# Performance work log

Measured on AMD Instinct MI355X. Metric: run time of the kernel, lower is better.

Reference implementation:

```python
import jax, jax.numpy as jnp
import numpy as np


def setup_inputs() -> dict:
    key = jax.random.key(0)
    k1, k2 = jax.random.split(key)
    B, D, H, W = 64, 64, 32, 32
    K = 1024
    z_e = jax.random.normal(k1, (B, D, H, W), dtype=jnp.float32)
    embedding = jax.random.normal(k2, (K, D), dtype=jnp.float32)
    return {"z_e": z_e, "embedding": embedding}


def reference(z_e, embedding):
    # Eval-mode forward of VectorQuantizer (EMA buffer updates are training-only state).
    B, D, H, W = z_e.shape
    K = embedding.shape[0]
    # (N, D) flattened encoder outputs, N = B*H*W
    flat = jnp.transpose(z_e, (0, 2, 3, 1)).reshape(-1, D)
    dist = (jnp.sum(flat * flat, axis=1, keepdims=True)
            + jnp.sum(embedding * embedding, axis=1)
            - 2.0 * flat @ embedding.T)  # (N, K)
    indices = jnp.argmin(dist, axis=1)  # (N,)
    z_q_flat = embedding[indices]  # (N, D) gather
    z_q = jnp.transpose(z_q_flat.reshape(B, H, W, D), (0, 3, 1, 2))
    # commitment loss: mse(z_e, sg(z_q))
    commitment_loss = jnp.mean((z_e - jax.lax.stop_gradient(z_q)) ** 2)
    # straight-through estimator
    z_q = z_e + jax.lax.stop_gradient(z_q - z_e)
    indices_bhw = indices.reshape(B, H, W)
    # fraction of codebook entries used this batch (jit-friendly unique count)
    used = jnp.zeros((K,), dtype=jnp.float32).at[indices].set(1.0)
    codebook_usage = jnp.sum(used) / K
    return z_q, commitment_loss, indices_bhw, codebook_usage
```

## Files before the change

kernel.cpp:

```cpp
#include <hip/hip_runtime.h>


#define DIMS 64
#define K_CODES 1024
#define N_QUERIES 65536
#define HW 1024
#define TOTAL_ELEMS 4194304
#define PLANE 4096

typedef __attribute__((ext_vector_type(8))) short v8s;
typedef __attribute__((ext_vector_type(4))) float f32x4;

__device__ inline unsigned short f2bf(float x) {
    union { float f; unsigned u; } v; v.f = x;
    unsigned r = v.u + 0x7fff + ((v.u >> 16) & 1);
    return (unsigned short)(r >> 16);
}
__device__ inline float bf2f(unsigned short h) {
    union { unsigned u; float f; } v; v.u = ((unsigned)h) << 16; return v.f;
}

__global__ void vq_prep(const float* __restrict__ emb, float* __restrict__ ws_norm,
                        int* __restrict__ ws_flags, float* __restrict__ ws_loss) {
    int k = blockIdx.x * 256 + threadIdx.x;
    const float4* row = (const float4*)(emb + k * DIMS);
    float s = 0.f;
#pragma unroll
    for (int i = 0; i < 16; ++i) {
        float4 v = row[i];
        s += v.x * v.x + v.y * v.y + v.z * v.z + v.w * v.w;
    }
    ws_norm[k] = s;
    ws_flags[k] = 0;
    if (k == 0) *ws_loss = 0.f;
}

#define MFMA16(A_, B_, C_) __builtin_amdgcn_mfma_f32_16x16x32_bf16(A_, B_, C_, 0, 0, 0)

__global__ __launch_bounds__(256, 2)
void vq_main(const float* __restrict__ z_e, const float* __restrict__ emb,
             const float* __restrict__ ws_norm, int* __restrict__ ws_flags,
             float* __restrict__ ws_loss, float* __restrict__ out) {
    __shared__ unsigned short ldsB[2][3 * PLANE];
    __shared__ int   fIdx[128];
    __shared__ float wsum[4];

    const int tid  = threadIdx.x;
    const int lane = tid & 63;
    const int wid  = tid >> 6;
    const int qbase = blockIdx.x * 128;
    const int b    = qbase >> 10;
    const int hwb  = qbase & (HW - 1);

    const int col  = lane & 15;
    const int qd   = lane >> 4;

    v8s afr[2][2][3];
    {
        const float* zb = z_e + b * (DIMS * HW);
#pragma unroll
        for (int rt = 0; rt < 2; ++rt) {
            int hwq = hwb + wid * 32 + rt * 16 + col;
#pragma unroll
            for (int kc = 0; kc < 2; ++kc) {
                int dbase = kc * 32 + qd * 8;
#pragma unroll
                for (int j = 0; j < 8; ++j) {
                    float x = zb[(dbase + j) * HW + hwq];
                    unsigned short h = f2bf(x);  float r1 = x - bf2f(h);
                    unsigned short m = f2bf(r1); float r2 = r1 - bf2f(m);
                    afr[rt][kc][0][j] = (short)h;
                    afr[rt][kc][1][j] = (short)m;
                    afr[rt][kc][2][j] = (short)f2bf(r2);
                }
            }
        }
    }

    float bestv[2][4];
    int   besti[2][4];
#pragma unroll
    for (int rt = 0; rt < 2; ++rt)
#pragma unroll
        for (int r = 0; r < 4; ++r) { bestv[rt][r] = 3.4e38f; besti[rt][r] = 0; }

    float4 regs[4];

    auto stage_loads = [&](int t) {
        const float4* src = (const float4*)(emb + t * 64 * DIMS);
#pragma unroll
        for (int i = 0; i < 4; ++i) regs[i] = src[tid + 256 * i];
    };
    auto stage_write = [&](int bb) {
        unsigned short* dst = &ldsB[bb][0];
#pragma unroll
        for (int i = 0; i < 4; ++i) {
            int e    = (tid + 256 * i) * 4;
            int code = e >> 6;
            int d    = e & 63;
            int o    = d >> 3;
            int sub  = d & 7;
            float xs[4] = {regs[i].x, regs[i].y, regs[i].z, regs[i].w};
            unsigned short h[4], mm_[4], l[4];
#pragma unroll
            for (int q = 0; q < 4; ++q) {
                float x = xs[q];
                unsigned short hh = f2bf(x);  float r1 = x - bf2f(hh);
                unsigned short mh = f2bf(r1); float r2 = r1 - bf2f(mh);
                h[q] = hh; mm_[q] = mh; l[q] = f2bf(r2);
            }
            int base = (o * 64 + code) * 8 + sub;
            uint2 uh, um, ul;
            uh.x = (unsigned)h[0]   | ((unsigned)h[1] << 16);
            uh.y = (unsigned)h[2]   | ((unsigned)h[3] << 16);
            um.x = (unsigned)mm_[0] | ((unsigned)mm_[1] << 16);
            um.y = (unsigned)mm_[2] | ((unsigned)mm_[3] << 16);
            ul.x = (unsigned)l[0]   | ((unsigned)l[1] << 16);
            ul.y = (unsigned)l[2]   | ((unsigned)l[3] << 16);
            *(uint2*)(dst + base)             = uh;
            *(uint2*)(dst + PLANE + base)     = um;
            *(uint2*)(dst + 2 * PLANE + base) = ul;
        }
    };

    stage_loads(0);
    stage_write(0);
    __syncthreads();

    for (int t = 0; t < 16; ++t) {
        const int cur = t & 1;
        if (t < 15) stage_loads(t + 1);
        const unsigned short* bufc = &ldsB[cur][0];
#pragma unroll
        for (int cs = 0; cs < 4; ++cs) {
            float nrm = ws_norm[t * 64 + cs * 16 + col];
            v8s bfr[2][3];
#pragma unroll
            for (int kc = 0; kc < 2; ++kc)
#pragma unroll
                for (int p = 0; p < 3; ++p)
                    bfr[kc][p] = *(const v8s*)(bufc + p * PLANE +
                                 (((kc * 4 + qd) * 64) + cs * 16 + col) * 8);
            f32x4 acc0 = {0.f, 0.f, 0.f, 0.f};
            f32x4 acc1 = {0.f, 0.f, 0.f, 0.f};
#pragma unroll
            for (int kc = 0; kc < 2; ++kc) {
                acc0 = MFMA16(afr[0][kc][0], bfr[kc][0], acc0);
                acc1 = MFMA16(afr[1][kc][0], bfr[kc][0], acc1);
                acc0 = MFMA16(afr[0][kc][0], bfr[kc][1], acc0);
                acc1 = MFMA16(afr[1][kc][0], bfr[kc][1], acc1);
                acc0 = MFMA16(afr[0][kc][1], bfr[kc][0], acc0);
                acc1 = MFMA16(afr[1][kc][1], bfr[kc][0], acc1);
                acc0 = MFMA16(afr[0][kc][1], bfr[kc][1], acc0);
                acc1 = MFMA16(afr[1][kc][1], bfr[kc][1], acc1);
                acc0 = MFMA16(afr[0][kc][0], bfr[kc][2], acc0);
                acc1 = MFMA16(afr[1][kc][0], bfr[kc][2], acc1);
                acc0 = MFMA16(afr[0][kc][2], bfr[kc][0], acc0);
                acc1 = MFMA16(afr[1][kc][2], bfr[kc][0], acc1);
            }
            int cbase = t * 64 + cs * 16 + col;
#pragma unroll
            for (int r = 0; r < 4; ++r) {
                float d0 = fmaf(-2.f, acc0[r], nrm);
                if (d0 < bestv[0][r]) { bestv[0][r] = d0; besti[0][r] = cbase; }
                float d1 = fmaf(-2.f, acc1[r], nrm);
                if (d1 < bestv[1][r]) { bestv[1][r] = d1; besti[1][r] = cbase; }
            }
        }
        if (t < 15) stage_write(1 - cur);
        __syncthreads();
    }

#pragma unroll
    for (int rt = 0; rt < 2; ++rt)
#pragma unroll
    for (int r = 0; r < 4; ++r) {
        float v = bestv[rt][r];
        int   idx = besti[rt][r];
#pragma unroll
        for (int m = 8; m >= 1; m >>= 1) {
            float ov = __shfl_xor(v, m, 64);
            int   oi = __shfl_xor(idx, m, 64);
            if (ov < v || (ov == v && oi < idx)) { v = ov; idx = oi; }
        }
        if (col == 0) {
            int q = wid * 32 + rt * 16 + qd * 4 + r;
            fIdx[q] = idx;
            out[TOTAL_ELEMS + 1 + qbase + q] = (float)idx;
            ws_flags[idx] = 1;
        }
    }
    __syncthreads();

    const int q  = tid & 127;
    const int dh = tid >> 7;
    const int n  = qbase + q;
    const int bb = n >> 10;
    const int hw = n & (HW - 1);
    const int myIdx = fIdx[q];
    const float* erow = emb + myIdx * DIMS;
    float lsum = 0.f;
#pragma unroll
    for (int it = 0; it < 32; ++it) {
        int d = it * 2 + dh;
        float v = erow[d];
        int   o = bb * (DIMS * HW) + d * HW + hw;
        float ze = z_e[o];
        out[o] = v;
        float df = ze - v;
        lsum = fmaf(df, df, lsum);
    }
#pragma unroll
    for (int off = 32; off > 0; off >>= 1) lsum += __shfl_down(lsum, off, 64);
    if (lane == 0) wsum[wid] = lsum;
    __syncthreads();
    if (tid == 0) atomicAdd(ws_loss, wsum[0] + wsum[1] + wsum[2] + wsum[3]);
}

__global__ void vq_final(const int* __restrict__ flags, const float* __restrict__ loss,
                         float* __restrict__ out) {
    __shared__ int cnt[256];
    int tid = threadIdx.x;
    int c = flags[tid] + flags[tid + 256] + flags[tid + 512] + flags[tid + 768];
    cnt[tid] = c;
    __syncthreads();
    for (int s = 128; s > 0; s >>= 1) {
        if (tid < s) cnt[tid] += cnt[tid + s];
        __syncthreads();
    }
    if (tid == 0) {
        out[TOTAL_ELEMS] = *loss / (float)TOTAL_ELEMS;
        out[TOTAL_ELEMS + 1 + N_QUERIES] = (float)cnt[0] / (float)K_CODES;
    }
}

extern "C" void kernel_launch(void* const* d_in, const int* in_sizes, int n_in,
                              void* d_out, int out_size, void* d_ws, size_t ws_size,
                              hipStream_t stream) {
    const float* z_e = (const float*)d_in[0];
    const float* emb = (const float*)d_in[1];
    float* out = (float*)d_out;
    float* ws_norm  = (float*)d_ws;
    int*   ws_flags = (int*)((char*)d_ws + 4096);
    float* ws_loss  = (float*)((char*)d_ws + 8192);

    vq_prep<<<4, 256, 0, stream>>>(emb, ws_norm, ws_flags, ws_loss);
    vq_main<<<512, 256, 0, stream>>>(z_e, emb, ws_norm, ws_flags, ws_loss, out);
    vq_final<<<1, 256, 0, stream>>>(ws_flags, ws_loss, out);
}
```

Measured before the change: 135.8 us.

## Precompute bf16 split codebook planes once and stream them via direct LDS loads

The prep kernel now splits the codebook into three bf16 planes in the MFMA-friendly layout once and stores them in workspace. The main kernel stages each tile with global_load_lds 16-byte copies instead of every block redoing the fp32 load and three-way split. This removes redundant conversion ALU work and register staging from the inner loop across 512 blocks. It also drops the final kernel: a last-block-done atomic counter computes the usage fraction and loss, at the cost of atomic traffic and a fence-based pattern.

```diff
diff --git a/kernel.cpp b/kernel.cpp
--- a/kernel.cpp
+++ b/kernel.cpp
@@ -3,10 +3,17 @@
 
 #define DIMS 64
 #define K_CODES 1024
-#define N_QUERIES 65536
+#define NQ 65536
 #define HW 1024
-#define TOTAL_ELEMS 4194304
+#define TOT 4194304
 #define PLANE 4096
+#define TILE_BYTES 24576
+
+#define WS_NORM   0
+#define WS_FLAGS  4096
+#define WS_LOSS   8192
+#define WS_CNT    8256
+#define WS_PLANES 16384
 
 typedef __attribute__((ext_vector_type(8))) short v8s;
 typedef __attribute__((ext_vector_type(4))) float f32x4;
@@ -19,31 +26,79 @@
 __device__ inline float bf2f(unsigned short h) {
     union { unsigned u; float f; } v; v.u = ((unsigned)h) << 16; return v.f;
 }
-
-__global__ void vq_prep(const float* __restrict__ emb, float* __restrict__ ws_norm,
-                        int* __restrict__ ws_flags, float* __restrict__ ws_loss) {
-    int k = blockIdx.x * 256 + threadIdx.x;
-    const float4* row = (const float4*)(emb + k * DIMS);
-    float s = 0.f;
-#pragma unroll
-    for (int i = 0; i < 16; ++i) {
-        float4 v = row[i];
-        s += v.x * v.x + v.y * v.y + v.z * v.z + v.w * v.w;
-    }
-    ws_norm[k] = s;
-    ws_flags[k] = 0;
-    if (k == 0) *ws_loss = 0.f;
+__device__ inline void cp16(void* lds, const void* g) {
+    __builtin_amdgcn_global_load_lds(
+        (const __attribute__((address_space(1))) void*)g,
+        (__attribute__((address_space(3))) void*)lds, 16, 0, 0);
 }
 
 #define MFMA16(A_, B_, C_) __builtin_amdgcn_mfma_f32_16x16x32_bf16(A_, B_, C_, 0, 0, 0)
+
+__global__ void vq_prep(const float* __restrict__ emb, char* __restrict__ ws) {
+    float* norms = (float*)(ws + WS_NORM);
+    int*   flags = (int*)(ws + WS_FLAGS);
+    unsigned short* planes = (unsigned short*)(ws + WS_PLANES);
+
+    const int tid = threadIdx.x;
+    const float4* src = (const float4*)emb;
+#pragma unroll
+    for (int i = 0; i < 4; ++i) {
+        int f4 = blockIdx.x * 1024 + i * 256 + tid;
+        int code = f4 >> 4;
+        int t    = code >> 6;
+        int c    = code & 63;
+        int o    = (f4 >> 1) & 7;
+        int sub  = (f4 & 1) * 4;
+        float4 v = src[f4];
+        float xs[4] = {v.x, v.y, v.z, v.w};
+        unsigned short h[4], m[4], l[4];
+#pragma unroll
+        for (int q = 0; q < 4; ++q) {
+            float x = xs[q];
+            unsigned short hh = f2bf(x);  float r1 = x - bf2f(hh);
+            unsigned short mh = f2bf(r1); float r2 = r1 - bf2f(mh);
+            h[q] = hh; m[q] = mh; l[q] = f2bf(r2);
+        }
+        unsigned short* base = planes + (size_t)t * 12288 + ((o * 64 + c) * 8 + sub);
+        uint2 uh, um, ul;
+        uh.x = (unsigned)h[0] | ((unsigned)h[1] << 16);
+        uh.y = (unsigned)h[2] | ((unsigned)h[3] << 16);
+        um.x = (unsigned)m[0] | ((unsigned)m[1] << 16);
+        um.y = (unsigned)m[2] | ((unsigned)m[3] << 16);
+        ul.x = (unsigned)l[0] | ((unsigned)l[1] << 16);
+        ul.y = (unsigned)l[2] | ((unsigned)l[3] << 16);
+        *(uint2*)(base)             = uh;
+        *(uint2*)(base + PLANE)     = um;
+        *(uint2*)(base + 2 * PLANE) = ul;
+    }
+    int g = blockIdx.x * 256 + tid;
+    if (g < K_CODES) {
+        const float4* row = (const float4*)(emb + g * DIMS);
+        float s = 0.f;
+#pragma unroll
+        for (int i = 0; i < 16; ++i) {
+            float4 v = row[i];
+            s += v.x * v.x + v.y * v.y + v.z * v.z + v.w * v.w;
+        }
+        norms[g] = s;
+        flags[g] = 0;
+    }
+    if (g == 0) { *(float*)(ws + WS_LOSS) = 0.f; *(int*)(ws + WS_CNT) = 0; }
+}
 
 __global__ __launch_bounds__(256, 2)
 void vq_main(const float* __restrict__ z_e, const float* __restrict__ emb,
-             const float* __restrict__ ws_norm, int* __restrict__ ws_flags,
-             float* __restrict__ ws_loss, float* __restrict__ out) {
+             char* __restrict__ ws, float* __restrict__ out) {
     __shared__ unsigned short ldsB[2][3 * PLANE];
     __shared__ int   fIdx[128];
     __shared__ float wsum[4];
+    __shared__ int   amLast;
+
+    const float* norms = (const float*)(ws + WS_NORM);
+    int*   flags   = (int*)(ws + WS_FLAGS);
+    float* ws_loss = (float*)(ws + WS_LOSS);
+    int*   ws_cnt  = (int*)(ws + WS_CNT);
+    const char* planes = (const char*)(ws + WS_PLANES);
 
     const int tid  = threadIdx.x;
     const int lane = tid & 63;
@@ -51,7 +106,6 @@
     const int qbase = blockIdx.x * 128;
     const int b    = qbase >> 10;
     const int hwb  = qbase & (HW - 1);
-
     const int col  = lane & 15;
     const int qd   = lane >> 4;
 
@@ -84,56 +138,24 @@
 #pragma unroll
         for (int r = 0; r < 4; ++r) { bestv[rt][r] = 3.4e38f; besti[rt][r] = 0; }
 
-    float4 regs[4];
-
-    auto stage_loads = [&](int t) {
-        const float4* src = (const float4*)(emb + t * 64 * DIMS);
-#pragma unroll
-        for (int i = 0; i < 4; ++i) regs[i] = src[tid + 256 * i];
+    auto stage = [&](int t, int buf) {
+        const char* g = planes + (size_t)t * TILE_BYTES + wid * 6144 + lane * 16;
+        char* l = ((char*)&ldsB[buf][0]) + wid * 6144;
+#pragma unroll
+        for (int c = 0; c < 6; ++c)
+            cp16(l + c * 1024, g + c * 1024);
     };
-    auto stage_write = [&](int bb) {
-        unsigned short* dst = &ldsB[bb][0];
-#pragma unroll
-        for (int i = 0; i < 4; ++i) {
-            int e    = (tid + 256 * i) * 4;
-            int code = e >> 6;
-            int d    = e & 63;
-            int o    = d >> 3;
-            int sub  = d & 7;
-            float xs[4] = {regs[i].x, regs[i].y, regs[i].z, regs[i].w};
-            unsigned short h[4], mm_[4], l[4];
-#pragma unroll
-            for (int q = 0; q < 4; ++q) {
-                float x = xs[q];
-                unsigned short hh = f2bf(x);  float r1 = x - bf2f(hh);
-                unsigned short mh = f2bf(r1); float r2 = r1 - bf2f(mh);
-                h[q] = hh; mm_[q] = mh; l[q] = f2bf(r2);
-            }
-            int base = (o * 64 + code) * 8 + sub;
-            uint2 uh, um, ul;
-            uh.x = (unsigned)h[0]   | ((unsigned)h[1] << 16);
-            uh.y = (unsigned)h[2]   | ((unsigned)h[3] << 16);
-            um.x = (unsigned)mm_[0] | ((unsigned)mm_[1] << 16);
-            um.y = (unsigned)mm_[2] | ((unsigned)mm_[3] << 16);
-            ul.x = (unsigned)l[0]   | ((unsigned)l[1] << 16);
-            ul.y = (unsigned)l[2]   | ((unsigned)l[3] << 16);
-            *(uint2*)(dst + base)             = uh;
-            *(uint2*)(dst + PLANE + base)     = um;
-            *(uint2*)(dst + 2 * PLANE + base) = ul;
-        }
-    };
-
-    stage_loads(0);
-    stage_write(0);
+
+    stage(0, 0);
     __syncthreads();
 
     for (int t = 0; t < 16; ++t) {
         const int cur = t & 1;
-        if (t < 15) stage_loads(t + 1);
+        if (t < 15) stage(t + 1, 1 - cur);
         const unsigned short* bufc = &ldsB[cur][0];
 #pragma unroll
         for (int cs = 0; cs < 4; ++cs) {
-            float nrm = ws_norm[t * 64 + cs * 16 + col];
+            float nrm = norms[t * 64 + cs * 16 + col];
             v8s bfr[2][3];
 #pragma unroll
             for (int kc = 0; kc < 2; ++kc)
@@ -167,7 +189,6 @@
                 if (d1 < bestv[1][r]) { bestv[1][r] = d1; besti[1][r] = cbase; }
             }
         }
-        if (t < 15) stage_write(1 - cur);
         __syncthreads();
     }
 
@@ -186,8 +207,8 @@
         if (col == 0) {
             int q = wid * 32 + rt * 16 + qd * 4 + r;
             fIdx[q] = idx;
-            out[TOTAL_ELEMS + 1 + qbase + q] = (float)idx;
-            ws_flags[idx] = 1;
+            out[TOT + 1 + qbase + q] = (float)idx;
+            atomicExch(&flags[idx], 1);
         }
     }
     __syncthreads();
@@ -214,23 +235,30 @@
     for (int off = 32; off > 0; off >>= 1) lsum += __shfl_down(lsum, off, 64);
     if (lane == 0) wsum[wid] = lsum;
     __syncthreads();
-    if (tid == 0) atomicAdd(ws_loss, wsum[0] + wsum[1] + wsum[2] + wsum[3]);
-}
-
-__global__ void vq_final(const int* __restrict__ flags, const float* __restrict__ loss,
-                         float* __restrict__ out) {
-    __shared__ int cnt[256];
-    int tid = threadIdx.x;
-    int c = flags[tid] + flags[tid + 256] + flags[tid + 512] + flags[tid + 768];
-    cnt[tid] = c;
-    __syncthreads();
-    for (int s = 128; s > 0; s >>= 1) {
-        if (tid < s) cnt[tid] += cnt[tid + s];
+    if (tid == 0) {
+        atomicAdd(ws_loss, wsum[0] + wsum[1] + wsum[2] + wsum[3]);
+        __threadfence();
+        int prev = atomicAdd(ws_cnt, 1);
+        amLast = (prev == (int)gridDim.x - 1);
+    }
+    __syncthreads();
+
+    if (amLast) {
+        __threadfence();
+        float c = 0.f;
+#pragma unroll
+        for (int i = 0; i < 4; ++i)
+            c += (float)atomicAdd(&flags[tid + 256 * i], 0);
+#pragma unroll
+        for (int off = 32; off > 0; off >>= 1) c += __shfl_down(c, off, 64);
+        if (lane == 0) wsum[wid] = c;
         __syncthreads();
-    }
-    if (tid == 0) {
-        out[TOTAL_ELEMS] = *loss / (float)TOTAL_ELEMS;
-        out[TOTAL_ELEMS + 1 + N_QUERIES] = (float)cnt[0] / (float)K_CODES;
+        if (tid == 0) {
+            float used = wsum[0] + wsum[1] + wsum[2] + wsum[3];
+            out[TOT + 1 + NQ] = used / (float)K_CODES;
+            float L = atomicAdd(ws_loss, 0.f);
+            out[TOT] = L / (float)TOT;
+        }
     }
 }
 
@@ -240,11 +268,8 @@
     const float* z_e = (const float*)d_in[0];
     const float* emb = (const float*)d_in[1];
     float* out = (float*)d_out;
-    float* ws_norm  = (float*)d_ws;
-    int*   ws_flags = (int*)((char*)d_ws + 4096);
-    float* ws_loss  = (float*)((char*)d_ws + 8192);
-
-    vq_prep<<<4, 256, 0, stream>>>(emb, ws_norm, ws_flags, ws_loss);
-    vq_main<<<512, 256, 0, stream>>>(z_e, emb, ws_norm, ws_flags, ws_loss, out);
-    vq_final<<<1, 256, 0, stream>>>(ws_flags, ws_loss, out);
-}
+    char* ws = (char*)d_ws;
+
+    vq_prep<<<16, 256, 0, stream>>>(emb, ws);
+    vq_main<<<512, 256, 0, stream>>>(z_e, emb, ws, out);
+}
```

Measured after the change: 153.8 us. 13.3% more time.
